# Kernel tuning notes

Measured on AMD Instinct MI355X. Metric: run time of the kernel, lower is better.

The kernel has to match this reference:

```python
import jax, jax.numpy as jnp
import numpy as np

N_HEAD = 9
HEAD_DIM = 64
KV_PER_HEAD = 21  # 189 // 9
ROPE_BASE = 10000.0


def _rotate_half(x):
    # matches torch: x1 = first half (floor), x2 = rest; cat(-x2, x1)
    h = x.shape[-1] // 2
    return jnp.concatenate([-x[..., h:], x[..., :h]], axis=-1)


def _rope_cos_sin(T, dtype):
    inv_freq = 1.0 / (ROPE_BASE ** (jnp.arange(0, KV_PER_HEAD, 2, dtype=jnp.float32) / KV_PER_HEAD))  # [11]
    t = jnp.arange(T, dtype=jnp.float32)
    freqs = jnp.einsum('i,j->ij', t, inv_freq)          # [T, 11]
    emb = jnp.concatenate([freqs, freqs], axis=-1)      # [T, 22]
    cos = jnp.cos(emb)[:, :KV_PER_HEAD].astype(dtype)   # [T, 21]
    sin = jnp.sin(emb)[:, :KV_PER_HEAD].astype(dtype)
    return cos, sin


def setup_inputs() -> dict:
    key = jax.random.key(0)
    ks = jax.random.split(key, 5)
    B, T, C = 4, 2048, 576
    kv_dim = 189
    s = 0.02
    return {
        'x': jax.random.normal(ks[0], (B, T, C), dtype=jnp.float32),
        'Wq': jax.random.normal(ks[1], (C, C), dtype=jnp.float32) * s,
        'Wk': jax.random.normal(ks[2], (C, kv_dim), dtype=jnp.float32) * s,
        'Wv': jax.random.normal(ks[3], (C, kv_dim), dtype=jnp.float32) * s,
        'Wo': jax.random.normal(ks[4], (C, C), dtype=jnp.float32) * s,
    }


def reference(x, Wq, Wk, Wv, Wo):
    B, T, C = x.shape
    q = (x @ Wq).reshape(B, T, N_HEAD, HEAD_DIM).transpose(0, 2, 1, 3)      # [B,H,T,64]
    k = (x @ Wk).reshape(B, T, N_HEAD, KV_PER_HEAD).transpose(0, 2, 1, 3)   # [B,H,T,21]
    v = (x @ Wv).reshape(B, T, N_HEAD, KV_PER_HEAD).transpose(0, 2, 1, 3)   # [B,H,T,21]

    cos, sin = _rope_cos_sin(T, x.dtype)  # [T,21] each, broadcasts over B,H
    k_rot = k * cos + _rotate_half(k) * sin
    q_part = q[..., :KV_PER_HEAD]
    q_rot_part = q_part * cos + _rotate_half(q_part) * sin
    # q dims >= KV_PER_HEAD never touch nonzero K, so only the first 21 dims matter
    scale = 1.0 / np.sqrt(HEAD_DIM)
    scores = jnp.einsum('bhqd,bhkd->bhqk', q_rot_part, k_rot) * scale       # [B,H,T,T]
    causal = jnp.tril(jnp.ones((T, T), dtype=bool))
    scores = jnp.where(causal, scores, -1e9)
    attn = jax.nn.softmax(scores, axis=-1)
    y_small = jnp.einsum('bhqk,bhkd->bhqd', attn, v)                        # [B,H,T,21]
    # zero-pad up to head_dim (matches k_pad/v_pad construction)
    y = jnp.pad(y_small, ((0, 0), (0, 0), (0, 0), (0, HEAD_DIM - KV_PER_HEAD)))
    y = y.transpose(0, 2, 1, 3).reshape(B, T, C)
    return y @ Wo
```

## Files before the change

kernel.cpp:

```cpp
#include <hip/hip_runtime.h>
#include <hip/hip_bf16.h>

typedef unsigned short u16;
typedef unsigned int u32;
typedef __attribute__((ext_vector_type(8))) short bf16x8;
typedef __attribute__((ext_vector_type(4))) float f32x4;
typedef __attribute__((ext_vector_type(4))) int i32x4;

#define N_HEADS 9
#define T_SEQ 2048
#define BATCH 4
#define CDIM 576
#define ROWS (BATCH * T_SEQ)
#define NBH (BATCH * N_HEADS)
#define PART_SLOT ((size_t)NBH * T_SEQ * 32)

__device__ __forceinline__ u16 f2bf(float f) {
    u32 u = __float_as_uint(f);
    u32 r = u + 0x7FFFu + ((u >> 16) & 1u);
    return (u16)(r >> 16);
}
__device__ __forceinline__ float bf2f(u16 u) { return __uint_as_float(((u32)u) << 16); }
__device__ __forceinline__ u32 cvt_pk_bf16(float lo, float hi) {
    u32 r;
    asm("v_cvt_pk_bf16_f32 %0, %1, %2" : "=v"(r) : "v"(lo), "v"(hi));
    return r;
}
__device__ __forceinline__ float exp2_raw(float x) {
    float r;
    asm("v_exp_f32 %0, %1" : "=v"(r) : "v"(x));
    return r;
}

__global__ __launch_bounds__(256) void prep_wt(const float* __restrict__ Wq, const float* __restrict__ Wk,
                                               const float* __restrict__ Wv, const float* __restrict__ Wo,
                                               u16* __restrict__ WcT, u16* __restrict__ WoSubT,
                                               float* __restrict__ cosT, float* __restrict__ sinT) {
    int idx = blockIdx.x * 256 + threadIdx.x;
    if (idx < 576 * 576) {
        int n = idx / 576, k = idx - n * 576;
        float v;
        if (n < 189)      v = Wq[(size_t)k * 576 + (n / 21) * 64 + (n % 21)];
        else if (n < 378) v = Wk[(size_t)k * 189 + (n - 189)];
        else if (n < 567) v = Wv[(size_t)k * 189 + (n - 378)];
        else              v = 0.f;
        WcT[(size_t)n * 576 + k] = f2bf(v);
    }
    if (idx < 576 * 192) {
        int n = idx / 192, k = idx - n * 192;
        float v = 0.f;
        if (k < 189) v = Wo[(size_t)((k / 21) * 64 + (k % 21)) * 576 + n];
        WoSubT[(size_t)n * 192 + k] = f2bf(v);
    }
    if (idx < T_SEQ * 21) {
        int t = idx / 21, d = idx - t * 21;
        int i = (d < 11) ? d : d - 11;
        float e = (2.0f * (float)i) / 21.0f;
        float invf = exp2f(-e * 13.287712379549449f);
        float ang = (float)t * invf;
        cosT[idx] = cosf(ang);
        sinT[idx] = sinf(ang);
    }
}


template <int AF32, int OUTF32>
__global__ __launch_bounds__(256) void gemm_mfma(const void* __restrict__ Av, const u16* __restrict__ BT,
                                                 void* __restrict__ Cout, int K, int lda, int ldbt, int ldc) {
    __shared__ u16 As[128][32];
    __shared__ u16 Bs[64][32];
    const int tid = threadIdx.x;
    const int lane = tid & 63, w = tid >> 6;
    const int m0 = (blockIdx.x & 63) * 128, n0 = (blockIdx.x >> 6) * 64;
    const int k15 = lane & 15, g = lane >> 4;

    const int arow = tid >> 1;
    const int ac0 = (tid & 1) * 2;
    const int brow = tid >> 2, bc = tid & 3;

    f32x4 zero = {0.f, 0.f, 0.f, 0.f};
    f32x4 acc[2][4];
#pragma unroll
    for (int hf = 0; hf < 2; hf++)
#pragma unroll
        for (int n = 0; n < 4; n++) acc[hf][n] = zero;

    const float* Af = (const float*)Av;
    const u16*   Ab = (const u16*)Av;

    float4 af0, af1, af2, af3;
    i32x4 av0, av1;
    if (AF32) {
        const float* ap = &Af[(size_t)(m0 + arow) * lda + ac0 * 8];
        af0 = *(const float4*)&ap[0];
        af1 = *(const float4*)&ap[4];
        af2 = *(const float4*)&ap[8];
        af3 = *(const float4*)&ap[12];
    } else {
        av0 = *(const i32x4*)&Ab[(size_t)(m0 + arow) * lda + ac0 * 8];
        av1 = *(const i32x4*)&Ab[(size_t)(m0 + arow) * lda + (ac0 + 1) * 8];
    }
    i32x4 bv = *(const i32x4*)&BT[(size_t)(n0 + brow) * ldbt + bc * 8];

    for (int k0 = 0; k0 < K; k0 += 32) {
        __syncthreads();
        if (AF32) {
            i32x4 w0, w1;
            w0[0] = (int)cvt_pk_bf16(af0.x, af0.y); w0[1] = (int)cvt_pk_bf16(af0.z, af0.w);
            w0[2] = (int)cvt_pk_bf16(af1.x, af1.y); w0[3] = (int)cvt_pk_bf16(af1.z, af1.w);
            w1[0] = (int)cvt_pk_bf16(af2.x, af2.y); w1[1] = (int)cvt_pk_bf16(af2.z, af2.w);
            w1[2] = (int)cvt_pk_bf16(af3.x, af3.y); w1[3] = (int)cvt_pk_bf16(af3.z, af3.w);
            *(i32x4*)&As[arow][(ac0 ^ (arow & 3)) * 8] = w0;
            *(i32x4*)&As[arow][((ac0 + 1) ^ (arow & 3)) * 8] = w1;
        } else {
            *(i32x4*)&As[arow][(ac0 ^ (arow & 3)) * 8] = av0;
            *(i32x4*)&As[arow][((ac0 + 1) ^ (arow & 3)) * 8] = av1;
        }
        *(i32x4*)&Bs[brow][(bc ^ (brow & 3)) * 8] = bv;
        __syncthreads();
        int k1 = k0 + 32;
        if (k1 < K) {
            if (AF32) {
                const float* ap = &Af[(size_t)(m0 + arow) * lda + k1 + ac0 * 8];
                af0 = *(const float4*)&ap[0];
                af1 = *(const float4*)&ap[4];
                af2 = *(const float4*)&ap[8];
                af3 = *(const float4*)&ap[12];
            } else {
                av0 = *(const i32x4*)&Ab[(size_t)(m0 + arow) * lda + k1 + ac0 * 8];
                av1 = *(const i32x4*)&Ab[(size_t)(m0 + arow) * lda + k1 + (ac0 + 1) * 8];
            }
            bv = *(const i32x4*)&BT[(size_t)(n0 + brow) * ldbt + k1 + bc * 8];
        }
        const int ar0 = w * 32 + k15;
        bf16x8 a0 = *(const bf16x8*)&As[ar0][(g ^ (ar0 & 3)) * 8];
        bf16x8 a1 = *(const bf16x8*)&As[ar0 + 16][(g ^ (ar0 & 3)) * 8];
#pragma unroll
        for (int n = 0; n < 4; n++) {
            int br = n * 16 + k15;
            bf16x8 b = *(const bf16x8*)&Bs[br][(g ^ (br & 3)) * 8];
            acc[0][n] = __builtin_amdgcn_mfma_f32_16x16x32_bf16(a0, b, acc[0][n], 0, 0, 0);
            acc[1][n] = __builtin_amdgcn_mfma_f32_16x16x32_bf16(a1, b, acc[1][n], 0, 0, 0);
        }
    }
#pragma unroll
    for (int hf = 0; hf < 2; hf++)
#pragma unroll
        for (int n = 0; n < 4; n++)
#pragma unroll
            for (int i = 0; i < 4; i++) {
                int row = m0 + w * 32 + hf * 16 + g * 4 + i;
                int col = n0 + n * 16 + k15;
                float v = acc[hf][n][i];
                if (OUTF32) ((float*)Cout)[(size_t)row * ldc + col] = v;
                else        ((u16*)Cout)[(size_t)row * ldc + col] = f2bf(v);
            }
}


__global__ __launch_bounds__(256) void repack_qkv(const u16* __restrict__ qkv,
                                                  const float* __restrict__ cosT,
                                                  const float* __restrict__ sinT,
                                                  u16* __restrict__ Qp, u16* __restrict__ Kp,
                                                  u16* __restrict__ Vp) {
    __shared__ u16 Qs[64][40];
    __shared__ u16 Ksh[64][40];
    __shared__ u16 Vsh[64][40];
    const int tid = threadIdx.x;
    const int bh = blockIdx.y;
    const int b = bh / N_HEADS, h = bh - b * N_HEADS;
    const int t0 = blockIdx.x * 64;

    const int qa = (h * 21) & ~7,        qoff = h * 21 - qa;
    const int ka = (189 + h * 21) & ~7,  koff = 189 + h * 21 - ka;
    const int va = (378 + h * 21) & ~7,  voff = 378 + h * 21 - va;

#pragma unroll
    for (int it = 0; it < 3; ++it) {
        int idx = tid + it * 256;
        int row = idx / 12;
        int r12 = idx - row * 12;
        int stream = r12 >> 2, chunk = r12 & 3;
        int off = (stream == 0) ? qa : (stream == 1) ? ka : va;
        const u16* src = qkv + (size_t)(b * T_SEQ + t0 + row) * CDIM + off + chunk * 8;
        i32x4 v = *(const i32x4*)src;
        u16* dst = (stream == 0) ? &Qs[row][0] : (stream == 1) ? &Ksh[row][0] : &Vsh[row][0];
        *(i32x4*)&dst[chunk * 8] = v;
    }
    __syncthreads();

    const int r = tid >> 2, c = tid & 3;
    const int t = t0 + r;
    const float* cr = cosT + t * 21;
    const float* sr = sinT + t * 21;
    u32 wq[4] = {0, 0, 0, 0}, wk[4] = {0, 0, 0, 0};
    const float sc = 0.18033688011112042f;
#pragma unroll
    for (int j = 0; j < 8; j++) {
        int d = c * 8 + j;
        float vq = 0.f, vk = 0.f;
        if (d < 21) {
            int pd = (d < 11) ? d + 10 : d - 11;
            float cc = cr[d], ss = sr[d];
            float qv = bf2f(Qs[r][qoff + d]),  qp = bf2f(Qs[r][qoff + pd]);
            float kv = bf2f(Ksh[r][koff + d]), kp = bf2f(Ksh[r][koff + pd]);
            float rq = (d < 11) ? -qp : qp;
            float rk = (d < 11) ? -kp : kp;
            vq = (qv * cc + rq * ss) * sc;
            vk = kv * cc + rk * ss;
        }
        wq[j >> 1] |= (u32)f2bf(vq) << ((j & 1) * 16);
        wk[j >> 1] |= (u32)f2bf(vk) << ((j & 1) * 16);
    }
    size_t obase = ((size_t)bh * T_SEQ + t) * 32 + c * 8;
    i32x4 q4; q4[0] = (int)wq[0]; q4[1] = (int)wq[1]; q4[2] = (int)wq[2]; q4[3] = (int)wq[3];
    i32x4 k4; k4[0] = (int)wk[0]; k4[1] = (int)wk[1]; k4[2] = (int)wk[2]; k4[3] = (int)wk[3];
    *(i32x4*)&Qp[obase] = q4;
    *(i32x4*)&Kp[obase] = k4;

    const int dv = tid >> 3, tc = tid & 7;
    u32 wv[4];
#pragma unroll
    for (int j = 0; j < 4; j++) {
        u16 lo, hi;
        if (dv < 21)      { lo = Vsh[tc * 8 + j * 2][voff + dv]; hi = Vsh[tc * 8 + j * 2 + 1][voff + dv]; }
        else if (dv == 31){ lo = 0x3F80; hi = 0x3F80; }
        else              { lo = 0; hi = 0; }
        wv[j] = (u32)lo | ((u32)hi << 16);
    }
    i32x4 v4; v4[0] = (int)wv[0]; v4[1] = (int)wv[1]; v4[2] = (int)wv[2]; v4[3] = (int)wv[3];
    *(i32x4*)&Vp[((size_t)bh * 32 + dv) * T_SEQ + t0 + tc * 8] = v4;
}


__global__ __launch_bounds__(256) void attn_mfma(const u16* __restrict__ Qp,
                                                 const u16* __restrict__ Kp,
                                                 const u16* __restrict__ Vp,
                                                 u16* __restrict__ Ybuf,
                                                 u16* __restrict__ Part) {
    __shared__ u16 Ks[128][40];
    __shared__ u16 Vt[32][136];
    __shared__ u16 Pt[2][4][16][72];
    const int tid = threadIdx.x;
    const int lane = tid & 63, w = tid >> 6;
    const int bh = blockIdx.y;
    const int b = bh / N_HEADS, h = bh - b * N_HEADS;
    const int k15 = lane & 15, g = lane >> 4;

    int bx = blockIdx.x, qt, ci;
    if (bx < 32)      { qt = 31 - (bx >> 2); ci = bx & 3; }
    else if (bx < 56) { int r = bx - 32; int q3 = r / 3; qt = 23 - q3; ci = r - q3 * 3; }
    else if (bx < 72) { int r = bx - 56; qt = 15 - (r >> 1); ci = r & 1; }
    else              { qt = 79 - bx; ci = 0; }
    const int q0 = qt * 64;
    const int n128 = (qt + 2) >> 1;
    const int nc = (qt >> 3) + 1;
    const int u_begin = (ci * n128) / nc;
    const int u_end = ((ci + 1) * n128) / nc;

    const u16* Kg = Kp + (((size_t)bh << 11) * 32) + (tid >> 1) * 32 + (tid & 1) * 16;
    const u16* Vg = Vp + (size_t)bh * 32 * T_SEQ + (size_t)(tid >> 3) * T_SEQ + (tid & 7) * 16;
    const int krow = tid >> 1, kcc = (tid & 1) * 16;
    const int vrow = tid >> 3, vcc = (tid & 7) * 16;

    bf16x8 qf = *(const bf16x8*)&Qp[(((size_t)bh << 11) + q0 + w * 16 + k15) * 32 + g * 8];

    f32x4 y0 = {0.f, 0.f, 0.f, 0.f}, y1 = {0.f, 0.f, 0.f, 0.f};
    const int qloc = w * 16 + k15;

    u32 ko = (u32)u_begin * 4096u;
    u32 vo = (u32)u_begin * 128u;
    i32x4 ka0 = *(const i32x4*)&Kg[ko];
    i32x4 ka1 = *(const i32x4*)&Kg[ko + 8];
    i32x4 va0 = *(const i32x4*)&Vg[vo];
    i32x4 va1 = *(const i32x4*)&Vg[vo + 8];

    for (int u = u_begin; u < u_end; ++u) {
        __syncthreads();
        *(i32x4*)&Ks[krow][kcc] = ka0;
        *(i32x4*)&Ks[krow][kcc + 8] = ka1;
        *(i32x4*)&Vt[vrow][vcc] = va0;
        *(i32x4*)&Vt[vrow][vcc + 8] = va1;
        if (u + 1 < u_end) {
            ko += 4096u; vo += 128u;
            ka0 = *(const i32x4*)&Kg[ko];
            ka1 = *(const i32x4*)&Kg[ko + 8];
            va0 = *(const i32x4*)&Vg[vo];
            va1 = *(const i32x4*)&Vg[vo + 8];
        }
        __syncthreads();

        const int kt0 = u * 2;
        const bool has1 = (kt0 + 1 <= qt);

        f32x4 s0[4], s1[4];
#pragma unroll
        for (int f = 0; f < 4; f++) {
            bf16x8 kf = *(const bf16x8*)&Ks[f * 16 + k15][g * 8];
            f32x4 z = {0.f, 0.f, 0.f, 0.f};
            s0[f] = __builtin_amdgcn_mfma_f32_16x16x32_bf16(kf, qf, z, 0, 0, 0);
        }
        if (has1) {
#pragma unroll
            for (int f = 0; f < 4; f++) {
                bf16x8 kf = *(const bf16x8*)&Ks[64 + f * 16 + k15][g * 8];
                f32x4 z = {0.f, 0.f, 0.f, 0.f};
                s1[f] = __builtin_amdgcn_mfma_f32_16x16x32_bf16(kf, qf, z, 0, 0, 0);
            }
        }
        if (kt0 == qt) {
#pragma unroll
            for (int f = 0; f < 4; f++)
#pragma unroll
                for (int i = 0; i < 4; i++)
                    if (f * 16 + g * 4 + i > qloc) s0[f][i] = -16384.f;
        }
        if (has1 && kt0 + 1 == qt) {
#pragma unroll
            for (int f = 0; f < 4; f++)
#pragma unroll
                for (int i = 0; i < 4; i++)
                    if (f * 16 + g * 4 + i > qloc) s1[f][i] = -16384.f;
        }

#pragma unroll
        for (int f = 0; f < 4; f++) {
            u32 lo = cvt_pk_bf16(exp2_raw(s0[f][0]), exp2_raw(s0[f][1]));
            u32 hi = cvt_pk_bf16(exp2_raw(s0[f][2]), exp2_raw(s0[f][3]));
            uint2 pk; pk.x = lo; pk.y = hi;
            *(uint2*)&Pt[0][w][k15][f * 16 + g * 4] = pk;
        }
        if (has1) {
#pragma unroll
            for (int f = 0; f < 4; f++) {
                u32 lo = cvt_pk_bf16(exp2_raw(s1[f][0]), exp2_raw(s1[f][1]));
                u32 hi = cvt_pk_bf16(exp2_raw(s1[f][2]), exp2_raw(s1[f][3]));
                uint2 pk; pk.x = lo; pk.y = hi;
                *(uint2*)&Pt[1][w][k15][f * 16 + g * 4] = pk;
            }
        }
        asm volatile("" ::: "memory");

#pragma unroll
        for (int kh = 0; kh < 2; kh++) {
            bf16x8 pa = *(const bf16x8*)&Pt[0][w][k15][kh * 32 + g * 8];
            bf16x8 v0 = *(const bf16x8*)&Vt[k15][kh * 32 + g * 8];
            bf16x8 v1 = *(const bf16x8*)&Vt[16 + k15][kh * 32 + g * 8];
            y0 = __builtin_amdgcn_mfma_f32_16x16x32_bf16(pa, v0, y0, 0, 0, 0);
            y1 = __builtin_amdgcn_mfma_f32_16x16x32_bf16(pa, v1, y1, 0, 0, 0);
        }
        if (has1) {
#pragma unroll
            for (int kh = 0; kh < 2; kh++) {
                bf16x8 pa = *(const bf16x8*)&Pt[1][w][k15][kh * 32 + g * 8];
                bf16x8 v0 = *(const bf16x8*)&Vt[k15][64 + kh * 32 + g * 8];
                bf16x8 v1 = *(const bf16x8*)&Vt[16 + k15][64 + kh * 32 + g * 8];
                y0 = __builtin_amdgcn_mfma_f32_16x16x32_bf16(pa, v0, y0, 0, 0, 0);
                y1 = __builtin_amdgcn_mfma_f32_16x16x32_bf16(pa, v1, y1, 0, 0, 0);
            }
        }
        asm volatile("" ::: "memory");
    }

    if (nc == 1) {
#pragma unroll
        for (int i = 0; i < 4; i++) {
            float li = __shfl(y1[i], (lane & 48) + 15);
            float inv = 1.0f / li;
            int rowY = b * T_SEQ + q0 + w * 16 + g * 4 + i;
            u16* yr = &Ybuf[(size_t)rowY * 192 + h * 21];
            yr[k15] = f2bf(y0[i] * inv);
            if (k15 < 5) yr[16 + k15] = f2bf(y1[i] * inv);
        }
    } else {
#pragma unroll
        for (int i = 0; i < 4; i++) {
            size_t pb = (size_t)ci * PART_SLOT +
                        (((size_t)bh << 11) + q0 + w * 16 + g * 4 + i) * 32;
            Part[pb + k15] = f2bf(y0[i]);
            Part[pb + 16 + k15] = f2bf(y1[i]);
        }
    }
}

__global__ __launch_bounds__(256) void attn_reduce(const u16* __restrict__ Part, u16* __restrict__ Ybuf) {
    int gid = blockIdx.x * 256 + threadIdx.x;
    int d = gid & 31;
    int rest = gid >> 5;
    int t = 512 + (rest % 1536);
    int bh = rest / 1536;
    int b = bh / N_HEADS, h = bh - b * N_HEADS;
    int qt = t >> 6;
    int nc = (qt >> 3) + 1;
    size_t base = (((size_t)bh << 11) + t) * 32;
    float l = 0.f, v = 0.f;
    for (int ci = 0; ci < nc; ci++) {
        l += bf2f(Part[(size_t)ci * PART_SLOT + base + 31]);
        if (d < 21) v += bf2f(Part[(size_t)ci * PART_SLOT + base + d]);
    }
    if (d < 21) Ybuf[(size_t)(b * T_SEQ + t) * 192 + h * 21 + d] = f2bf(v / l);
}


extern "C" void kernel_launch(void* const* d_in, const int* in_sizes, int n_in,
                              void* d_out, int out_size, void* d_ws, size_t ws_size,
                              hipStream_t stream) {
    const float* x  = (const float*)d_in[0];
    const float* Wq = (const float*)d_in[1];
    const float* Wk = (const float*)d_in[2];
    const float* Wv = (const float*)d_in[3];
    const float* Wo = (const float*)d_in[4];
    float* out = (float*)d_out;

    char* p = (char*)d_ws;
    auto alloc = [&](size_t bytes) { char* r = p; p += (bytes + 255) & ~(size_t)255; return r; };
    u16*   QpKp   = (u16*)alloc((size_t)ROWS * CDIM * 2);
    u16*   qkv    = (u16*)alloc((size_t)ROWS * CDIM * 2);
    u16*   WcT    = (u16*)alloc((size_t)576 * 576 * 2);
    u16*   WoSubT = (u16*)alloc((size_t)576 * 192 * 2);
    float* cosT   = (float*)alloc((size_t)T_SEQ * 21 * 4);
    float* sinT   = (float*)alloc((size_t)T_SEQ * 21 * 4);
    u16*   Vp     = (u16*)alloc((size_t)NBH * 32 * T_SEQ * 2);
    u16*   Ybuf   = (u16*)alloc((size_t)ROWS * 192 * 2);
    u16*   Part   = (u16*)alloc((size_t)4 * PART_SLOT * 2);

    u16* Qp = QpKp;
    u16* Kp = QpKp + (size_t)NBH * T_SEQ * 32;

    prep_wt<<<dim3((576 * 576 + 255) / 256), dim3(256), 0, stream>>>(Wq, Wk, Wv, Wo, WcT, WoSubT, cosT, sinT);

    gemm_mfma<1, 0><<<dim3(64 * 9), dim3(256), 0, stream>>>((const void*)x, WcT, (void*)qkv, 576, 576, 576, 576);

    repack_qkv<<<dim3(T_SEQ / 64, NBH), dim3(256), 0, stream>>>(qkv, cosT, sinT, Qp, Kp, Vp);

    attn_mfma<<<dim3(80, NBH), dim3(256), 0, stream>>>(Qp, Kp, Vp, Ybuf, Part);
    attn_reduce<<<dim3(NBH * 1536 * 32 / 256), dim3(256), 0, stream>>>(Part, Ybuf);

    gemm_mfma<0, 1><<<dim3(64 * 9), dim3(256), 0, stream>>>((const void*)Ybuf, WoSubT, (void*)out, 192, 192, 192, 576);
}
```

Measured before the change: 79.83 us.

## Use 128-row query tiles with 8 waves sharing each K/V tile load

Each attention block now covers 128 query rows with 512 threads (8 waves), so every K/V tile staged in shared memory serves twice as many queries. Loading is split: the first 256 threads fetch K and the rest fetch V. Per-wave predicates skip the key tiles that lie above the causal diagonal. The grid is halved and the split-KV chunk mapping is recomputed for the larger tiles, which cuts global K/V traffic and the number of blocks. In exchange there is more divergence at the diagonal, fewer blocks to balance load, and larger blocks that may lower occupancy.

```diff
diff --git a/kernel.cpp b/kernel.cpp
--- a/kernel.cpp
+++ b/kernel.cpp
@@ -233,74 +233,80 @@
 }
 
 
-__global__ __launch_bounds__(256) void attn_mfma(const u16* __restrict__ Qp,
+__global__ __launch_bounds__(512) void attn_mfma(const u16* __restrict__ Qp,
                                                  const u16* __restrict__ Kp,
                                                  const u16* __restrict__ Vp,
                                                  u16* __restrict__ Ybuf,
                                                  u16* __restrict__ Part) {
     __shared__ u16 Ks[128][40];
     __shared__ u16 Vt[32][136];
-    __shared__ u16 Pt[2][4][16][72];
+    __shared__ u16 Pt[2][8][16][72];
     const int tid = threadIdx.x;
     const int lane = tid & 63, w = tid >> 6;
     const int bh = blockIdx.y;
     const int b = bh / N_HEADS, h = bh - b * N_HEADS;
     const int k15 = lane & 15, g = lane >> 4;
 
-    int bx = blockIdx.x, qt, ci;
-    if (bx < 32)      { qt = 31 - (bx >> 2); ci = bx & 3; }
-    else if (bx < 56) { int r = bx - 32; int q3 = r / 3; qt = 23 - q3; ci = r - q3 * 3; }
-    else if (bx < 72) { int r = bx - 56; qt = 15 - (r >> 1); ci = r & 1; }
-    else              { qt = 79 - bx; ci = 0; }
-    const int q0 = qt * 64;
-    const int n128 = (qt + 2) >> 1;
-    const int nc = (qt >> 3) + 1;
+    int qt2 = 15, ci = blockIdx.x;
+    for (int q = 15; q >= 0; --q) {
+        int n = (q >> 2) + 1;
+        if (ci < n) { qt2 = q; break; }
+        ci -= n;
+    }
+    const int q0 = qt2 * 128;
+    const int n128 = qt2 + 1;
+    const int nc = (qt2 >> 2) + 1;
     const int u_begin = (ci * n128) / nc;
     const int u_end = ((ci + 1) * n128) / nc;
 
-    const u16* Kg = Kp + (((size_t)bh << 11) * 32) + (tid >> 1) * 32 + (tid & 1) * 16;
-    const u16* Vg = Vp + (size_t)bh * 32 * T_SEQ + (size_t)(tid >> 3) * T_SEQ + (tid & 7) * 16;
-    const int krow = tid >> 1, kcc = (tid & 1) * 16;
-    const int vrow = tid >> 3, vcc = (tid & 7) * 16;
+    const bool isK = (tid < 256);
+    const int krow = (tid & 255) >> 2, kc = tid & 3;
+    const int vrow = (tid & 255) >> 3, vc = tid & 7;
+    const u16* Kg = Kp + (size_t)bh * 65536 + krow * 32 + kc * 8;
+    const u16* Vg = Vp + (size_t)bh * 65536 + vrow * 2048 + vc * 8;
 
     bf16x8 qf = *(const bf16x8*)&Qp[(((size_t)bh << 11) + q0 + w * 16 + k15) * 32 + g * 8];
 
     f32x4 y0 = {0.f, 0.f, 0.f, 0.f}, y1 = {0.f, 0.f, 0.f, 0.f};
-    const int qloc = w * 16 + k15;
-
-    u32 ko = (u32)u_begin * 4096u;
-    u32 vo = (u32)u_begin * 128u;
-    i32x4 ka0 = *(const i32x4*)&Kg[ko];
-    i32x4 ka1 = *(const i32x4*)&Kg[ko + 8];
-    i32x4 va0 = *(const i32x4*)&Vg[vo];
-    i32x4 va1 = *(const i32x4*)&Vg[vo + 8];
+    const int qloc = (w & 3) * 16 + k15;
+    const int kd = 2 * qt2 + (w >> 2);
+
+    u32 off = (u32)u_begin * 4096u;
+    u32 voffu = (u32)u_begin * 128u;
+    i32x4 r0, r1;
+    if (isK) { r0 = *(const i32x4*)&Kg[off];   r1 = *(const i32x4*)&Kg[off + 2048]; }
+    else     { r0 = *(const i32x4*)&Vg[voffu]; r1 = *(const i32x4*)&Vg[voffu + 64]; }
 
     for (int u = u_begin; u < u_end; ++u) {
         __syncthreads();
-        *(i32x4*)&Ks[krow][kcc] = ka0;
-        *(i32x4*)&Ks[krow][kcc + 8] = ka1;
-        *(i32x4*)&Vt[vrow][vcc] = va0;
-        *(i32x4*)&Vt[vrow][vcc + 8] = va1;
+        if (isK) {
+            *(i32x4*)&Ks[krow][kc * 8] = r0;
+            *(i32x4*)&Ks[krow + 64][kc * 8] = r1;
+        } else {
+            *(i32x4*)&Vt[vrow][vc * 8] = r0;
+            *(i32x4*)&Vt[vrow][vc * 8 + 64] = r1;
+        }
         if (u + 1 < u_end) {
-            ko += 4096u; vo += 128u;
-            ka0 = *(const i32x4*)&Kg[ko];
-            ka1 = *(const i32x4*)&Kg[ko + 8];
-            va0 = *(const i32x4*)&Vg[vo];
-            va1 = *(const i32x4*)&Vg[vo + 8];
+            off += 4096u; voffu += 128u;
+            if (isK) { r0 = *(const i32x4*)&Kg[off];   r1 = *(const i32x4*)&Kg[off + 2048]; }
+            else     { r0 = *(const i32x4*)&Vg[voffu]; r1 = *(const i32x4*)&Vg[voffu + 64]; }
         }
         __syncthreads();
 
         const int kt0 = u * 2;
-        const bool has1 = (kt0 + 1 <= qt);
+        const bool do0 = (kt0 <= kd);
+        const bool do1 = (kt0 + 1 <= kd);
 
         f32x4 s0[4], s1[4];
-#pragma unroll
-        for (int f = 0; f < 4; f++) {
-            bf16x8 kf = *(const bf16x8*)&Ks[f * 16 + k15][g * 8];
-            f32x4 z = {0.f, 0.f, 0.f, 0.f};
-            s0[f] = __builtin_amdgcn_mfma_f32_16x16x32_bf16(kf, qf, z, 0, 0, 0);
-        }
-        if (has1) {
+        if (do0) {
+#pragma unroll
+            for (int f = 0; f < 4; f++) {
+                bf16x8 kf = *(const bf16x8*)&Ks[f * 16 + k15][g * 8];
+                f32x4 z = {0.f, 0.f, 0.f, 0.f};
+                s0[f] = __builtin_amdgcn_mfma_f32_16x16x32_bf16(kf, qf, z, 0, 0, 0);
+            }
+        }
+        if (do1) {
 #pragma unroll
             for (int f = 0; f < 4; f++) {
                 bf16x8 kf = *(const bf16x8*)&Ks[64 + f * 16 + k15][g * 8];
@@ -308,14 +314,14 @@
                 s1[f] = __builtin_amdgcn_mfma_f32_16x16x32_bf16(kf, qf, z, 0, 0, 0);
             }
         }
-        if (kt0 == qt) {
+        if (do0 && kt0 == kd) {
 #pragma unroll
             for (int f = 0; f < 4; f++)
 #pragma unroll
                 for (int i = 0; i < 4; i++)
                     if (f * 16 + g * 4 + i > qloc) s0[f][i] = -16384.f;
         }
-        if (has1 && kt0 + 1 == qt) {
+        if (do1 && kt0 + 1 == kd) {
 #pragma unroll
             for (int f = 0; f < 4; f++)
 #pragma unroll
@@ -323,14 +329,16 @@
                     if (f * 16 + g * 4 + i > qloc) s1[f][i] = -16384.f;
         }
 
-#pragma unroll
-        for (int f = 0; f < 4; f++) {
-            u32 lo = cvt_pk_bf16(exp2_raw(s0[f][0]), exp2_raw(s0[f][1]));
-            u32 hi = cvt_pk_bf16(exp2_raw(s0[f][2]), exp2_raw(s0[f][3]));
-            uint2 pk; pk.x = lo; pk.y = hi;
-            *(uint2*)&Pt[0][w][k15][f * 16 + g * 4] = pk;
-        }
-        if (has1) {
+        if (do0) {
+#pragma unroll
+            for (int f = 0; f < 4; f++) {
+                u32 lo = cvt_pk_bf16(exp2_raw(s0[f][0]), exp2_raw(s0[f][1]));
+                u32 hi = cvt_pk_bf16(exp2_raw(s0[f][2]), exp2_raw(s0[f][3]));
+                uint2 pk; pk.x = lo; pk.y = hi;
+                *(uint2*)&Pt[0][w][k15][f * 16 + g * 4] = pk;
+            }
+        }
+        if (do1) {
 #pragma unroll
             for (int f = 0; f < 4; f++) {
                 u32 lo = cvt_pk_bf16(exp2_raw(s1[f][0]), exp2_raw(s1[f][1]));
@@ -341,15 +349,17 @@
         }
         asm volatile("" ::: "memory");
 
-#pragma unroll
-        for (int kh = 0; kh < 2; kh++) {
-            bf16x8 pa = *(const bf16x8*)&Pt[0][w][k15][kh * 32 + g * 8];
-            bf16x8 v0 = *(const bf16x8*)&Vt[k15][kh * 32 + g * 8];
-            bf16x8 v1 = *(const bf16x8*)&Vt[16 + k15][kh * 32 + g * 8];
-            y0 = __builtin_amdgcn_mfma_f32_16x16x32_bf16(pa, v0, y0, 0, 0, 0);
-            y1 = __builtin_amdgcn_mfma_f32_16x16x32_bf16(pa, v1, y1, 0, 0, 0);
-        }
-        if (has1) {
+        if (do0) {
+#pragma unroll
+            for (int kh = 0; kh < 2; kh++) {
+                bf16x8 pa = *(const bf16x8*)&Pt[0][w][k15][kh * 32 + g * 8];
+                bf16x8 v0 = *(const bf16x8*)&Vt[k15][kh * 32 + g * 8];
+                bf16x8 v1 = *(const bf16x8*)&Vt[16 + k15][kh * 32 + g * 8];
+                y0 = __builtin_amdgcn_mfma_f32_16x16x32_bf16(pa, v0, y0, 0, 0, 0);
+                y1 = __builtin_amdgcn_mfma_f32_16x16x32_bf16(pa, v1, y1, 0, 0, 0);
+            }
+        }
+        if (do1) {
 #pragma unroll
             for (int kh = 0; kh < 2; kh++) {
                 bf16x8 pa = *(const bf16x8*)&Pt[1][w][k15][kh * 32 + g * 8];
@@ -390,8 +400,7 @@
     int t = 512 + (rest % 1536);
     int bh = rest / 1536;
     int b = bh / N_HEADS, h = bh - b * N_HEADS;
-    int qt = t >> 6;
-    int nc = (qt >> 3) + 1;
+    int nc = (t >> 9) + 1;
     size_t base = (((size_t)bh << 11) + t) * 32;
     float l = 0.f, v = 0.f;
     for (int ci = 0; ci < nc; ci++) {
@@ -433,7 +442,7 @@
 
     repack_qkv<<<dim3(T_SEQ / 64, NBH), dim3(256), 0, stream>>>(qkv, cosT, sinT, Qp, Kp, Vp);
 
-    attn_mfma<<<dim3(80, NBH), dim3(256), 0, stream>>>(Qp, Kp, Vp, Ybuf, Part);
+    attn_mfma<<<dim3(40, NBH), dim3(512), 0, stream>>>(Qp, Kp, Vp, Ybuf, Part);
     attn_reduce<<<dim3(NBH * 1536 * 32 / 256), dim3(256), 0, stream>>>(Part, Ybuf);
 
     gemm_mfma<0, 1><<<dim3(64 * 9), dim3(256), 0, stream>>>((const void*)Ybuf, WoSubT, (void*)out, 192, 192, 192, 576);
```

New measurement: 77.73 us, median of 3. 1.03x faster.
